# Optimization experiments

Measured on AMD Instinct MI355X. Metric: run time of the kernel, lower is better.

Reference implementation:

```python
import jax, jax.numpy as jnp
import numpy as np

BUCKET_SIZE = 64
N_HASHES = 8


def setup_inputs() -> dict:
    key = jax.random.key(0)
    ks = jax.random.split(key, 8)
    B, S, D = 4, 4096, 512
    n_buckets = S // BUCKET_SIZE  # 64
    x = jax.random.normal(ks[0], (B, S, D), dtype=jnp.float32)
    rotations = jax.random.normal(ks[1], (1, D, N_HASHES, n_buckets // 2), dtype=jnp.float32)
    w_qk = jax.random.normal(ks[2], (D, D), dtype=jnp.float32) * 0.02
    b_qk = jax.random.normal(ks[3], (D,), dtype=jnp.float32) * 0.02
    w_v = jax.random.normal(ks[4], (D, D), dtype=jnp.float32) * 0.02
    b_v = jax.random.normal(ks[5], (D,), dtype=jnp.float32) * 0.02
    w_out = jax.random.normal(ks[6], (D, D), dtype=jnp.float32) * 0.02
    b_out = jax.random.normal(ks[7], (D,), dtype=jnp.float32) * 0.02
    return {"x": x, "rotations": rotations, "w_qk": w_qk, "b_qk": b_qk,
            "w_v": w_v, "b_v": b_v, "w_out": w_out, "b_out": b_out}


def reference(x, rotations, w_qk, b_qk, w_v, b_v, w_out, b_out):
    B, S, D = x.shape
    T = S  # seqlen is already a multiple of 2*bucket_size -> no padding
    n_buckets = T // BUCKET_SIZE
    qk = x @ w_qk + b_qk            # [B, T, D]
    v = x @ w_v + b_v               # [B, T, D]

    # --- LSH bucketing ---
    rot = jnp.einsum('btf,fhi->bhti', qk, rotations[0])      # [B, H, T, nb/2]
    rot = jnp.concatenate([rot, -rot], axis=-1)              # [B, H, T, nb]
    buckets = jnp.argmax(rot, axis=-1)                       # [B, H, T]
    offsets = (jnp.arange(N_HASHES) * n_buckets)[None, :, None]
    buckets = (buckets + offsets).reshape(B, -1)             # [B, H*T]

    # --- stable sort by (bucket, position) ---
    ticker = jnp.arange(N_HASHES * T)[None, :]
    buckets_and_t = T * buckets + ticker % T                 # unique keys
    sticker = jnp.argsort(buckets_and_t, axis=-1)            # sorted ticker values
    undo_sort = jnp.argsort(sticker, axis=-1)
    st = sticker % T                                         # token positions

    # --- gather Q/K/V into sorted order ---
    idx = jnp.broadcast_to(st[:, :, None], (B, N_HASHES * T, D))
    sqk = jnp.take_along_axis(qk, idx, axis=1)               # [B, H*T, D]
    sv = jnp.take_along_axis(v, idx, axis=1)

    # --- chunked attention (no softmax, as in the original module) ---
    chunks = N_HASHES * n_buckets
    bq = sqk.reshape(B, chunks, BUCKET_SIZE, D)
    bv = sv.reshape(B, chunks, BUCKET_SIZE, D)
    norm = jnp.maximum(jnp.linalg.norm(bq, axis=-1, keepdims=True), 1e-12)
    bk = bq / norm                                           # F.normalize(p=2)
    dots = jnp.einsum('buie,buje->buij', bq, bk) * (D ** -0.5)
    bo = jnp.einsum('buij,buje->buie', dots, bv)             # [B, chunks, bs, D]

    # --- scatter back and combine hash rounds ---
    so = bo.reshape(B, -1, D)
    uidx = jnp.broadcast_to(undo_sort[:, :, None], (B, N_HASHES * T, D))
    o = jnp.take_along_axis(so, uidx, axis=1)
    out = o.reshape(B, N_HASHES, T, D).sum(axis=1)           # sum over hash rounds
    return out @ w_out + b_out
```

## Files before the change

kernel.cpp:

```cpp
#include <hip/hip_runtime.h>


typedef __attribute__((ext_vector_type(8))) short short8;
typedef __attribute__((ext_vector_type(4))) float f32x4;
typedef unsigned short ushort_t;

__device__ __forceinline__ ushort_t f2b(float f) {
  union { float f; unsigned u; } x; x.f = f;
  unsigned r = x.u + 0x7fffu + ((x.u >> 16) & 1u);
  return (ushort_t)(r >> 16);
}
__device__ __forceinline__ float b2f(unsigned b) {
  union { unsigned u; float f; } x; x.u = b << 16;
  return x.f;
}
__device__ __forceinline__ void gload16(void* lds, const void* gp) {
  __builtin_amdgcn_global_load_lds(
      (const __attribute__((address_space(1))) unsigned int*)gp,
      (__attribute__((address_space(3))) unsigned int*)lds, 16, 0, 0);
}

__global__ __launch_bounds__(256) void prep_kernel(
    const float* __restrict__ x, const float* __restrict__ w_qk,
    const float* __restrict__ b_qk, const float* __restrict__ R,
    const float* __restrict__ w_v, const float* __restrict__ w_out,
    ushort_t* __restrict__ xh, ushort_t* __restrict__ xl,
    ushort_t* __restrict__ wqkT, ushort_t* __restrict__ wvT, ushort_t* __restrict__ woT,
    ushort_t* __restrict__ W2Th, ushort_t* __restrict__ W2Tl, float* __restrict__ b2,
    int* __restrict__ mcount)
{
  __shared__ float t[32][33];
  __shared__ float wrow[512];
  const int blk = blockIdx.x, tid = threadIdx.x;
  if (blk == 0 && tid == 0) mcount[0] = 0;

  if (blk < 4096) {
    const int i = blk * 256 + tid;
    const float4 a = *(const float4*)(x + (size_t)i * 8);
    const float4 c = *(const float4*)(x + (size_t)i * 8 + 4);
    float v[8] = { a.x, a.y, a.z, a.w, c.x, c.y, c.z, c.w };
    ushort_t hi[8], lo[8];
    #pragma unroll
    for (int k = 0; k < 8; ++k) {
      hi[k] = f2b(v[k]);
      lo[k] = f2b(v[k] - b2f(hi[k]));
    }
    *(uint4*)(xh + (size_t)i * 8) = *(const uint4*)hi;
    *(uint4*)(xl + (size_t)i * 8) = *(const uint4*)lo;
  } else if (blk < 4864) {
    const int idx = blk - 4096;
    const int mat = idx >> 8, r = idx & 255;
    const float* W  = (mat == 0) ? w_qk : (mat == 1) ? w_v : w_out;
    ushort_t*   Wt  = (mat == 0) ? wqkT : (mat == 1) ? wvT : woT;
    const int bx = (r & 15) * 32, by = (r >> 4) * 32;
    const int tx = tid & 31, ty = tid >> 5;
    #pragma unroll
    for (int j = 0; j < 4; ++j)
      t[ty + j*8][tx] = W[(size_t)(by + ty + j*8) * 512 + bx + tx];
    __syncthreads();
    #pragma unroll
    for (int j = 0; j < 4; ++j)
      Wt[(size_t)(bx + ty + j*8) * 512 + by + tx] = f2b(t[tx][ty + j*8]);
  } else {
    const int e = blk - 4864, j = tid;
    const float* src = (e < 512) ? (w_qk + (size_t)e * 512) : b_qk;
    wrow[j]       = src[j];
    wrow[j + 256] = src[j + 256];
    __syncthreads();
    float acc = 0.f;
    for (int f = 0; f < 512; ++f)
      acc = fmaf(wrow[f], R[(size_t)f * 256 + j], acc);
    if (e < 512) {
      const ushort_t hi = f2b(acc);
      W2Th[(size_t)j * 512 + e] = hi;
      W2Tl[(size_t)j * 512 + e] = f2b(acc - b2f(hi));
    } else {
      b2[j] = acc;
    }
  }
}

__global__ __launch_bounds__(256, 2) void gemm_qkv(
    const ushort_t* __restrict__ A, const ushort_t* __restrict__ wqkT,
    const ushort_t* __restrict__ wvT, const float* __restrict__ b_qk,
    const float* __restrict__ b_v, ushort_t* __restrict__ qkv)
{
  __shared__ __align__(16) char Al[32768];
  __shared__ __align__(16) char Bl[32768];
  const int bm = blockIdx.x * 128;
  const int sel = blockIdx.y >> 2;
  const int bn = (blockIdx.y & 3) * 128;
  const ushort_t* Wt   = sel ? wvT : wqkT;
  const float*    bias = sel ? b_v : b_qk;
  const int coff = sel * 512;
  const int tid = threadIdx.x, w = tid >> 6, l = tid & 63;
  const int m = l & 15, gq = l >> 4;
  f32x4 acc[2][8] = {};

#define STAGE1(NB, K0) { \
    _Pragma("unroll") \
    for (int j = 0; j < 4; ++j) { \
      const int row = w * 32 + j * 8 + (l >> 3); \
      const int ch = (l & 7) ^ (row & 7); \
      const int dst = (NB) * 16384 + w * 4096 + j * 1024 + l * 16; \
      gload16(Al + dst, A  + (size_t)(bm + row) * 512 + (K0) + ch * 8); \
      gload16(Bl + dst, Wt + (size_t)(bn + row) * 512 + (K0) + ch * 8); \
    } }

  STAGE1(0, 0)
  __syncthreads();
  for (int t = 0; t < 8; ++t) {
    const int cur = t & 1;
    if (t < 7) STAGE1(cur ^ 1, (t + 1) * 64)
    #pragma unroll
    for (int ks = 0; ks < 2; ++ks) {
      short8 bfr[8];
      #pragma unroll
      for (int tj = 0; tj < 8; ++tj) {
        const int brow = tj * 16 + m;
        bfr[tj] = *(const short8*)(Bl + cur * 16384 + ((brow * 128 + ks * 64 + gq * 16) ^ ((brow & 7) << 4)));
      }
      #pragma unroll
      for (int ti = 0; ti < 2; ++ti) {
        const int arow = w * 32 + ti * 16 + m;
        const short8 af = *(const short8*)(Al + cur * 16384 + ((arow * 128 + ks * 64 + gq * 16) ^ ((arow & 7) << 4)));
        #pragma unroll
        for (int tj = 0; tj < 8; ++tj)
          acc[ti][tj] = __builtin_amdgcn_mfma_f32_16x16x32_bf16(af, bfr[tj], acc[ti][tj], 0, 0, 0);
      }
    }
    __syncthreads();
  }
#undef STAGE1
  #pragma unroll
  for (int ti = 0; ti < 2; ++ti)
    #pragma unroll
    for (int tj = 0; tj < 8; ++tj) {
      const int col = bn + tj * 16 + m;
      const float bvv = bias[col];
      #pragma unroll
      for (int r2 = 0; r2 < 4; ++r2) {
        const int row = bm + w * 32 + ti * 16 + gq * 4 + r2;
        qkv[(size_t)row * 1024 + coff + col] = f2b(acc[ti][tj][r2] + bvv);
      }
    }
}

__global__ __launch_bounds__(256, 2) void gemm_mfma(
    const ushort_t* __restrict__ A, const ushort_t* __restrict__ Wt,
    const float* __restrict__ bias, float* __restrict__ Cf)
{
  __shared__ __align__(16) char Al[32768];
  __shared__ __align__(16) char Bl[32768];
  const int bm = blockIdx.x * 128, bn = blockIdx.y * 128;
  const int tid = threadIdx.x, w = tid >> 6, l = tid & 63;
  const int m = l & 15, gq = l >> 4;
  f32x4 acc[2][8] = {};

#define STAGE1(NB, K0) { \
    _Pragma("unroll") \
    for (int j = 0; j < 4; ++j) { \
      const int row = w * 32 + j * 8 + (l >> 3); \
      const int ch = (l & 7) ^ (row & 7); \
      const int dst = (NB) * 16384 + w * 4096 + j * 1024 + l * 16; \
      gload16(Al + dst, A  + (size_t)(bm + row) * 512 + (K0) + ch * 8); \
      gload16(Bl + dst, Wt + (size_t)(bn + row) * 512 + (K0) + ch * 8); \
    } }

  STAGE1(0, 0)
  __syncthreads();
  for (int t = 0; t < 8; ++t) {
    const int cur = t & 1;
    if (t < 7) STAGE1(cur ^ 1, (t + 1) * 64)
    #pragma unroll
    for (int ks = 0; ks < 2; ++ks) {
      short8 bfr[8];
      #pragma unroll
      for (int tj = 0; tj < 8; ++tj) {
        const int brow = tj * 16 + m;
        bfr[tj] = *(const short8*)(Bl + cur * 16384 + ((brow * 128 + ks * 64 + gq * 16) ^ ((brow & 7) << 4)));
      }
      #pragma unroll
      for (int ti = 0; ti < 2; ++ti) {
        const int arow = w * 32 + ti * 16 + m;
        const short8 af = *(const short8*)(Al + cur * 16384 + ((arow * 128 + ks * 64 + gq * 16) ^ ((arow & 7) << 4)));
        #pragma unroll
        for (int tj = 0; tj < 8; ++tj)
          acc[ti][tj] = __builtin_amdgcn_mfma_f32_16x16x32_bf16(af, bfr[tj], acc[ti][tj], 0, 0, 0);
      }
    }
    __syncthreads();
  }
#undef STAGE1
  #pragma unroll
  for (int ti = 0; ti < 2; ++ti)
    #pragma unroll
    for (int tj = 0; tj < 8; ++tj) {
      const int col = bn + tj * 16 + m;
      const float bvv = bias[col];
      #pragma unroll
      for (int r2 = 0; r2 < 4; ++r2) {
        const int row = bm + w * 32 + ti * 16 + gq * 4 + r2;
        Cf[(size_t)row * 512 + col] = acc[ti][tj][r2] + bvv;
      }
    }
}

__global__ __launch_bounds__(256, 2) void rot3_mfma(
    const ushort_t* __restrict__ Ah, const ushort_t* __restrict__ Al,
    const ushort_t* __restrict__ Bh, const ushort_t* __restrict__ Bl,
    const float* __restrict__ b2, float* __restrict__ rot)
{
  __shared__ __align__(16) char AH[16384], AL[16384], BH[16384], BL[16384];
  const int bm = blockIdx.x * 128, bn = blockIdx.y * 128;
  const int tid = threadIdx.x, w = tid >> 6, l = tid & 63;
  const int m = l & 15, gq = l >> 4;
  f32x4 acc[2][8] = {};
  for (int k0 = 0; k0 < 512; k0 += 64) {
    #pragma unroll
    for (int j = 0; j < 4; ++j) {
      const int row = w * 32 + j * 8 + (l >> 3);
      const int ch = (l & 7) ^ (row & 7);
      const int dst = w * 4096 + j * 1024 + l * 16;
      gload16(AH + dst, Ah + (size_t)(bm + row) * 512 + k0 + ch * 8);
      gload16(AL + dst, Al + (size_t)(bm + row) * 512 + k0 + ch * 8);
      gload16(BH + dst, Bh + (size_t)(bn + row) * 512 + k0 + ch * 8);
      gload16(BL + dst, Bl + (size_t)(bn + row) * 512 + k0 + ch * 8);
    }
    __syncthreads();
    #pragma unroll
    for (int ks = 0; ks < 2; ++ks) {
      short8 bh8[8], bl8[8];
      #pragma unroll
      for (int tj = 0; tj < 8; ++tj) {
        const int ba = ((tj * 16 + m) * 128 + ks * 64 + gq * 16) ^ (((tj * 16 + m) & 7) << 4);
        bh8[tj] = *(const short8*)(BH + ba);
        bl8[tj] = *(const short8*)(BL + ba);
      }
      #pragma unroll
      for (int ti = 0; ti < 2; ++ti) {
        const int arow = w * 32 + ti * 16 + m;
        const int aa = (arow * 128 + ks * 64 + gq * 16) ^ ((arow & 7) << 4);
        const short8 ah8 = *(const short8*)(AH + aa);
        const short8 al8 = *(const short8*)(AL + aa);
        #pragma unroll
        for (int tj = 0; tj < 8; ++tj) {
          acc[ti][tj] = __builtin_amdgcn_mfma_f32_16x16x32_bf16(ah8, bh8[tj], acc[ti][tj], 0, 0, 0);
          acc[ti][tj] = __builtin_amdgcn_mfma_f32_16x16x32_bf16(al8, bh8[tj], acc[ti][tj], 0, 0, 0);
          acc[ti][tj] = __builtin_amdgcn_mfma_f32_16x16x32_bf16(ah8, bl8[tj], acc[ti][tj], 0, 0, 0);
        }
      }
    }
    __syncthreads();
  }
  #pragma unroll
  for (int ti = 0; ti < 2; ++ti)
    #pragma unroll
    for (int tj = 0; tj < 8; ++tj) {
      const int col = bn + tj * 16 + m;
      const float bvv = b2[col];
      #pragma unroll
      for (int r2 = 0; r2 < 4; ++r2) {
        const int row = bm + w * 32 + ti * 16 + gq * 4 + r2;
        rot[(size_t)row * 256 + col] = acc[ti][tj][r2] + bvv;
      }
    }
}

__global__ __launch_bounds__(256) void argmax_scale(
    const float* __restrict__ rot, int* __restrict__ buckets,
    int* __restrict__ mlist, int* __restrict__ mcount, float tau,
    const ushort_t* __restrict__ qkv, float* __restrict__ scale)
{
  const int blk = blockIdx.x;
  if (blk < 16384) {
    const int tok = blk;
    const int j = threadIdx.x;
    const float r = rot[(size_t)tok * 256 + j];
    float m1, m2; int i1;
    if (r >= 0.f) { m1 = r;  i1 = j & 31;        m2 = -r; }
    else          { m1 = -r; i1 = (j & 31) + 32; m2 = r;  }
    #pragma unroll
    for (int off = 16; off; off >>= 1) {
      const float om1 = __shfl_xor(m1, off);
      const int   oi1 = __shfl_xor(i1, off);
      const float om2 = __shfl_xor(m2, off);
      float loser;
      if (om1 > m1 || (om1 == m1 && oi1 < i1)) { loser = m1; m1 = om1; i1 = oi1; }
      else loser = om1;
      m2 = fmaxf(fmaxf(m2, om2), loser);
    }
    if ((j & 31) == 0) {
      const int h = j >> 5, b = tok >> 12, t = tok & 4095;
      buckets[((b << 3) + h) * 4096 + t] = i1;
      if (m1 - m2 < tau) {
        const int k = atomicAdd(mcount, 1);
        mlist[k] = (((b << 3) + h) << 12) | t;
      }
    }
  } else {
    const int wave = threadIdx.x >> 6, lane = threadIdx.x & 63;
    const int tok = (blk - 16384) * 4 + wave;
    const uint4 H = *(const uint4*)(qkv + (size_t)tok * 1024 + lane * 8);
    const unsigned* hp = (const unsigned*)&H;
    float s = 0.f;
    #pragma unroll
    for (int e = 0; e < 4; ++e) {
      const float v0 = b2f(hp[e] & 0xffffu);
      const float v1 = b2f(hp[e] >> 16);
      s += v0 * v0 + v1 * v1;
    }
    #pragma unroll
    for (int off = 32; off; off >>= 1) s += __shfl_down(s, off);
    if (lane == 0) {
      const float nn = fmaxf(sqrtf(s), 1e-12f);
      scale[tok] = 0.044194173824159216f / nn;
    }
  }
}

__global__ __launch_bounds__(512) void bucket_fallback(
    const float* __restrict__ x, const float* __restrict__ w_qk,
    const float* __restrict__ b_qk, const float* __restrict__ R,
    const int* __restrict__ mlist, const int* __restrict__ mcount,
    int* __restrict__ buckets)
{
  __shared__ float qkrow[512];
  const int n = mcount[0];
  for (int ii = blockIdx.x; ii < n; ii += gridDim.x) {
    const int mm = mlist[ii];
    const int bh = mm >> 12, t = mm & 4095;
    const int b = bh >> 3, h = bh & 7;
    const float* xr = x + ((size_t)b * 4096 + t) * 512;
    {
      const int c = threadIdx.x;
      float a0 = 0.f;
      for (int f = 0; f < 512; ++f) a0 = fmaf(xr[f], w_qk[(size_t)f * 512 + c], a0);
      qkrow[c] = a0 + b_qk[c];
    }
    __syncthreads();
    if (threadIdx.x < 32) {
      const int col = h * 32 + threadIdx.x;
      float a0 = 0.f;
      for (int f = 0; f < 512; ++f) a0 = fmaf(qkrow[f], R[(size_t)f * 256 + col], a0);
      float m1; int i1;
      if (a0 >= 0.f) { m1 = a0;  i1 = threadIdx.x; }
      else           { m1 = -a0; i1 = threadIdx.x + 32; }
      #pragma unroll
      for (int off = 16; off; off >>= 1) {
        const float om = __shfl_xor(m1, off);
        const int   oi = __shfl_xor(i1, off);
        if (om > m1 || (om == m1 && oi < i1)) { m1 = om; i1 = oi; }
      }
      if (threadIdx.x == 0) buckets[(size_t)bh * 4096 + t] = i1;
    }
    __syncthreads();
  }
}

__global__ __launch_bounds__(256) void sort_kernel(
    const int* __restrict__ buckets, int* __restrict__ st)
{
  __shared__ int bk_lds[4096];
  __shared__ int cnt[64][64];
  __shared__ int bstart[64];
  const int tid = threadIdx.x;
  const int base = blockIdx.x * 4096;
  const int wave = tid >> 6, lane = tid & 63;
  const unsigned long long lt = (1ull << lane) - 1ull;

  for (int t = tid; t < 4096; t += 256) bk_lds[t] = buckets[base + t];
  for (int i = tid; i < 4096; i += 256) ((int*)cnt)[i] = 0;
  __syncthreads();

  for (int c = wave; c < 64; c += 4) {
    const int bk = bk_lds[c * 64 + lane];
    unsigned long long mask = ~0ull;
    #pragma unroll
    for (int bit = 0; bit < 6; ++bit) {
      const unsigned long long bb = __ballot((bk >> bit) & 1);
      mask &= ((bk >> bit) & 1) ? bb : ~bb;
    }
    if ((mask & lt) == 0)
      cnt[c][bk] = __popcll(mask);
  }
  __syncthreads();

  if (tid < 64) {
    int run = 0;
    for (int c = 0; c < 64; ++c) {
      const int v = cnt[c][tid];
      cnt[c][tid] = run;
      run += v;
    }
    int ex = run;
    #pragma unroll
    for (int off = 1; off < 64; off <<= 1) {
      const int nn = __shfl_up(ex, off);
      if (lane >= off) ex += nn;
    }
    bstart[tid] = ex - run;
  }
  __syncthreads();

  for (int c = wave; c < 64; c += 4) {
    const int tok = c * 64 + lane;
    const int bk = bk_lds[tok];
    unsigned long long mask = ~0ull;
    #pragma unroll
    for (int bit = 0; bit < 6; ++bit) {
      const unsigned long long bb = __ballot((bk >> bit) & 1);
      mask &= ((bk >> bit) & 1) ? bb : ~bb;
    }
    const int rank = (int)__popcll(mask & lt);
    st[base + bstart[bk] + cnt[c][bk] + rank] = tok;
  }
}

__global__ __launch_bounds__(256, 2) void attn_mfma(
    const ushort_t* __restrict__ qkv, const float* __restrict__ scale,
    const int* __restrict__ st, ushort_t* __restrict__ so, int g, int hbase)
{
  __shared__ __align__(16) char Q[32768];
  __shared__ __align__(16) char VT[32768];
  __shared__ __align__(16) char P[8192];
  __shared__ int   stt[64];
  __shared__ float scl[64];

  const int blk = blockIdx.x;
  const int cpg = g * 64;
  const int b = blk / cpg, rem = blk % cpg;
  const int hl = rem >> 6, c = rem & 63;
  const int tid = threadIdx.x, w = tid >> 6, l = tid & 63;
  const int m = l & 15, gq = l >> 4;
  const int srow = tid >> 5, su = tid & 31;

  if (tid < 64) {
    const int s = st[(size_t)((b * 8 + hbase + hl) * 4096) + c * 64 + tid];
    stt[tid] = s;
    scl[tid] = scale[b * 4096 + s];
  }
  __syncthreads();

  const size_t qkbase = (size_t)b * 4096;
  uint4 rg[8];

#define LOADG(VOFF, HALF) { \
    _Pragma("unroll") \
    for (int it = 0; it < 8; ++it) { \
      const int row = it * 8 + srow; \
      rg[it] = *(const uint4*)(qkv + (qkbase + stt[row]) * 1024 + (VOFF) + (HALF) * 256 + su * 8); \
    } }
#define WRITEQ() { \
    _Pragma("unroll") \
    for (int it = 0; it < 8; ++it) { \
      const int row = it * 8 + srow; \
      *(uint4*)(Q + ((row * 512 + su * 16) ^ ((row & 7) << 4))) = rg[it]; \
    } }
#define WRITEVT() { \
    _Pragma("unroll") \
    for (int it = 0; it < 8; ++it) { \
      const int j = it * 8 + srow; \
      const ushort_t* e = (const ushort_t*)&rg[it]; \
      _Pragma("unroll") \
      for (int ee = 0; ee < 8; ++ee) { \
        const int d = su * 8 + ee; \
        *(ushort_t*)(VT + ((d * 128 + j * 2) ^ (((d ^ (d >> 3)) & 7) << 4))) = e[ee]; \
      } \
    } }
#define COMPUTE_S() { \
    _Pragma("unroll") \
    for (int kf = 0; kf < 8; ++kf) { \
      const int arow = w * 16 + m; \
      const short8 af = *(const short8*)(Q + ((arow * 512 + kf * 64 + gq * 16) ^ ((arow & 7) << 4))); \
      _Pragma("unroll") \
      for (int jt = 0; jt < 4; ++jt) { \
        const int brow = jt * 16 + m; \
        const short8 bf = *(const short8*)(Q + ((brow * 512 + kf * 64 + gq * 16) ^ ((brow & 7) << 4))); \
        accS[jt] = __builtin_amdgcn_mfma_f32_16x16x32_bf16(af, bf, accS[jt], 0, 0, 0); \
      } \
    } }
#define COMPUTE_PV(ACCO) { \
    _Pragma("unroll") \
    for (int dt = 0; dt < 16; ++dt) { \
      _Pragma("unroll") \
      for (int kf = 0; kf < 2; ++kf) { \
        const int d = dt * 16 + m; \
        const short8 bv = *(const short8*)(VT + ((d * 128 + kf * 64 + gq * 16) ^ (((d ^ (d >> 3)) & 7) << 4))); \
        ACCO[dt] = __builtin_amdgcn_mfma_f32_16x16x32_bf16(ap[kf], bv, ACCO[dt], 0, 0, 0); \
      } \
    } }
#define BOUNCE(ACCO) { \
    _Pragma("unroll") \
    for (int dt = 0; dt < 16; ++dt) \
      _Pragma("unroll") \
      for (int r = 0; r < 4; ++r) { \
        const int i = w * 16 + gq * 4 + r; \
        const int dcol = dt * 16 + m; \
        *(ushort_t*)(Q + ((i * 512 + dcol * 2) ^ ((i & 7) << 4))) = f2b(ACCO[dt][r]); \
      } }
#define FLUSH(HALF) { \
    _Pragma("unroll") \
    for (int it = 0; it < 8; ++it) { \
      const int row = it * 8 + srow; \
      const uint4 dat = *(const uint4*)(Q + ((row * 512 + su * 16) ^ ((row & 7) << 4))); \
      *(uint4*)(so + (sobase + stt[row]) * 512 + (HALF) * 256 + su * 8) = dat; \
    } }

  f32x4 accS[4] = {};

  LOADG(0, 0)
  WRITEQ()
  __syncthreads();
  LOADG(0, 1)
  COMPUTE_S()
  __syncthreads();
  WRITEQ()
  __syncthreads();
  LOADG(512, 0)
  COMPUTE_S()
  __syncthreads();

  #pragma unroll
  for (int jt = 0; jt < 4; ++jt)
    #pragma unroll
    for (int r = 0; r < 4; ++r) {
      const int i = w * 16 + gq * 4 + r;
      const int j = jt * 16 + m;
      *(ushort_t*)(P + ((i * 128 + j * 2) ^ ((i & 7) << 4))) = f2b(accS[jt][r] * scl[j]);
    }
  WRITEVT()
  __syncthreads();

  const size_t sobase = (size_t)(b * g + hl) * 4096;
  LOADG(512, 1)
  short8 ap[2];
  #pragma unroll
  for (int kf = 0; kf < 2; ++kf) {
    const int i = w * 16 + m;
    ap[kf] = *(const short8*)(P + ((i * 128 + kf * 64 + gq * 16) ^ ((i & 7) << 4)));
  }
  f32x4 accO[16] = {};
  COMPUTE_PV(accO)
  __syncthreads();

  WRITEVT()
  BOUNCE(accO)
  __syncthreads();

  FLUSH(0)
  f32x4 accO2[16] = {};
  COMPUTE_PV(accO2)
  __syncthreads();

  BOUNCE(accO2)
  __syncthreads();
  FLUSH(1)

#undef LOADG
#undef WRITEQ
#undef WRITEVT
#undef COMPUTE_S
#undef COMPUTE_PV
#undef BOUNCE
#undef FLUSH
}

__global__ __launch_bounds__(256) void gather_kernel(
    const ushort_t* __restrict__ so, ushort_t* __restrict__ o_b, int g, int first)
{
  const int tok = blockIdx.x;
  const int b = tok >> 12, t = tok & 4095;
  const int d0 = threadIdx.x * 2;
  ushort_t* dst = o_b + (size_t)tok * 512 + d0;
  float ax = 0.f, ay = 0.f;
  if (!first) {
    const unsigned u = *(const unsigned*)dst;
    ax = b2f(u & 0xffffu); ay = b2f(u >> 16);
  }
  const size_t stride = (size_t)4096 * 512;
  const ushort_t* src = so + ((size_t)(b * g) * 4096 + t) * 512 + d0;
  for (int hlp = 0; hlp < g; ++hlp) {
    const unsigned u = *(const unsigned*)src;
    ax += b2f(u & 0xffffu);
    ay += b2f(u >> 16);
    src += stride;
  }
  *(unsigned*)dst = ((unsigned)f2b(ay) << 16) | (unsigned)f2b(ax);
}

extern "C" void kernel_launch(void* const* d_in, const int* in_sizes, int n_in,
                              void* d_out, int out_size, void* d_ws, size_t ws_size,
                              hipStream_t stream) {
  const float* x         = (const float*)d_in[0];
  const float* rotations = (const float*)d_in[1];
  const float* w_qk      = (const float*)d_in[2];
  const float* b_qk      = (const float*)d_in[3];
  const float* w_v       = (const float*)d_in[4];
  const float* b_v       = (const float*)d_in[5];
  const float* w_out     = (const float*)d_in[6];
  const float* b_out     = (const float*)d_in[7];
  float* out = (float*)d_out;
  char* ws = (char*)d_ws;

  ushort_t* xh      = (ushort_t*)(ws);
  ushort_t* xl      = (ushort_t*)(ws + 16777216);
  ushort_t* qkv     = (ushort_t*)(ws + 33554432);
  float*    rot     = (float*)(ws + 67108864);
  ushort_t* o_b     = (ushort_t*)(ws + 67108864);
  ushort_t* wqkTh   = (ushort_t*)(ws + 83886080);
  ushort_t* wvT     = (ushort_t*)(ws + 84410368);
  ushort_t* woT     = (ushort_t*)(ws + 84934656);
  ushort_t* W2Th    = (ushort_t*)(ws + 85458944);
  ushort_t* W2Tl    = (ushort_t*)(ws + 85721088);
  float*    b2      = (float*)(ws + 85983232);
  float*    scale   = (float*)(ws + 85987328);
  int*      buckets = (int*)(ws + 86052864);
  int*      st      = (int*)(ws + 86577152);
  int*      mlist   = (int*)(ws + 87101440);
  int*      mcount  = (int*)(ws + 87625728);
  ushort_t* so      = (ushort_t*)(ws + 87629824);
  const size_t so_off = 87629824;

  int g = 1;
  for (int cand = 8; cand >= 1; cand >>= 1)
    if (so_off + (size_t)cand * 16777216ull <= ws_size) { g = cand; break; }

  const dim3 blk256(256);
  hipLaunchKernelGGL(prep_kernel, dim3(5377), blk256, 0, stream,
                     x, w_qk, b_qk, rotations, w_v, w_out,
                     xh, xl, wqkTh, wvT, woT, W2Th, W2Tl, b2, mcount);

  hipLaunchKernelGGL(gemm_qkv, dim3(128, 8), blk256, 0, stream, xh, wqkTh, wvT, b_qk, b_v, qkv);
  hipLaunchKernelGGL(rot3_mfma, dim3(128, 2), blk256, 0, stream, xh, xl, W2Th, W2Tl, b2, rot);

  hipLaunchKernelGGL(argmax_scale, dim3(20480), blk256, 0, stream,
                     rot, buckets, mlist, mcount, 1.5e-3f, qkv, scale);
  hipLaunchKernelGGL(bucket_fallback, dim3(1024), dim3(512), 0, stream,
                     x, w_qk, b_qk, rotations, mlist, mcount, buckets);
  hipLaunchKernelGGL(sort_kernel, dim3(32), blk256, 0, stream, buckets, st);

  const int passes = 8 / g;
  for (int p = 0; p < passes; ++p) {
    const int hbase = p * g;
    hipLaunchKernelGGL(attn_mfma, dim3(4 * g * 64), blk256, 0, stream,
                       qkv, scale, st, so, g, hbase);
    hipLaunchKernelGGL(gather_kernel, dim3(16384), blk256, 0, stream,
                       so, o_b, g, (p == 0) ? 1 : 0);
  }

  hipLaunchKernelGGL(gemm_mfma, dim3(128, 4), blk256, 0, stream, o_b, woT, b_out, out);
}
```

Before: 244.4 us.

## Merge QKV and rotation GEMMs into one launch; raise MFMA wave priority in attention

The QKV projection GEMM and the split-precision rotation GEMM now run as one kernel with a 128x10 grid. The first eight grid rows do the QKV tiles and the last two do the rotation tiles, sharing one 64KB LDS buffer. This removes a kernel launch and lets the small rotation GEMM (256 blocks) overlap with the QKV blocks instead of running as a separate under-filled wave. Separately, the attention kernel brackets its MFMA loops with s_setprio so waves issuing matrix ops get scheduling priority over waves doing loads.

```diff
diff --git a/kernel.cpp b/kernel.cpp
--- a/kernel.cpp
+++ b/kernel.cpp
@@ -80,22 +80,28 @@
   }
 }
 
-__global__ __launch_bounds__(256, 2) void gemm_qkv(
-    const ushort_t* __restrict__ A, const ushort_t* __restrict__ wqkT,
-    const ushort_t* __restrict__ wvT, const float* __restrict__ b_qk,
-    const float* __restrict__ b_v, ushort_t* __restrict__ qkv)
-{
-  __shared__ __align__(16) char Al[32768];
-  __shared__ __align__(16) char Bl[32768];
+__global__ __launch_bounds__(256, 2) void gemm_qkvr(
+    const ushort_t* __restrict__ A, const ushort_t* __restrict__ Axl,
+    const ushort_t* __restrict__ wqkT, const ushort_t* __restrict__ wvT,
+    const float* __restrict__ b_qk, const float* __restrict__ b_v,
+    ushort_t* __restrict__ qkv,
+    const ushort_t* __restrict__ W2Th, const ushort_t* __restrict__ W2Tl,
+    const float* __restrict__ b2, float* __restrict__ rot)
+{
+  __shared__ __align__(16) char lds[65536];
   const int bm = blockIdx.x * 128;
-  const int sel = blockIdx.y >> 2;
-  const int bn = (blockIdx.y & 3) * 128;
-  const ushort_t* Wt   = sel ? wvT : wqkT;
-  const float*    bias = sel ? b_v : b_qk;
-  const int coff = sel * 512;
   const int tid = threadIdx.x, w = tid >> 6, l = tid & 63;
   const int m = l & 15, gq = l >> 4;
-  f32x4 acc[2][8] = {};
+
+  if (blockIdx.y < 8) {
+    char* Al = lds;
+    char* Bl = lds + 32768;
+    const int sel = blockIdx.y >> 2;
+    const int bn = (blockIdx.y & 3) * 128;
+    const ushort_t* Wt   = sel ? wvT : wqkT;
+    const float*    bias = sel ? b_v : b_qk;
+    const int coff = sel * 512;
+    f32x4 acc[2][8] = {};
 
 #define STAGE1(NB, K0) { \
     _Pragma("unroll") \
@@ -107,43 +113,100 @@
       gload16(Bl + dst, Wt + (size_t)(bn + row) * 512 + (K0) + ch * 8); \
     } }
 
-  STAGE1(0, 0)
-  __syncthreads();
-  for (int t = 0; t < 8; ++t) {
-    const int cur = t & 1;
-    if (t < 7) STAGE1(cur ^ 1, (t + 1) * 64)
-    #pragma unroll
-    for (int ks = 0; ks < 2; ++ks) {
-      short8 bfr[8];
+    STAGE1(0, 0)
+    __syncthreads();
+    for (int t = 0; t < 8; ++t) {
+      const int cur = t & 1;
+      if (t < 7) STAGE1(cur ^ 1, (t + 1) * 64)
+      #pragma unroll
+      for (int ks = 0; ks < 2; ++ks) {
+        short8 bfr[8];
+        #pragma unroll
+        for (int tj = 0; tj < 8; ++tj) {
+          const int brow = tj * 16 + m;
+          bfr[tj] = *(const short8*)(Bl + cur * 16384 + ((brow * 128 + ks * 64 + gq * 16) ^ ((brow & 7) << 4)));
+        }
+        #pragma unroll
+        for (int ti = 0; ti < 2; ++ti) {
+          const int arow = w * 32 + ti * 16 + m;
+          const short8 af = *(const short8*)(Al + cur * 16384 + ((arow * 128 + ks * 64 + gq * 16) ^ ((arow & 7) << 4)));
+          #pragma unroll
+          for (int tj = 0; tj < 8; ++tj)
+            acc[ti][tj] = __builtin_amdgcn_mfma_f32_16x16x32_bf16(af, bfr[tj], acc[ti][tj], 0, 0, 0);
+        }
+      }
+      __syncthreads();
+    }
+#undef STAGE1
+    #pragma unroll
+    for (int ti = 0; ti < 2; ++ti)
       #pragma unroll
       for (int tj = 0; tj < 8; ++tj) {
-        const int brow = tj * 16 + m;
-        bfr[tj] = *(const short8*)(Bl + cur * 16384 + ((brow * 128 + ks * 64 + gq * 16) ^ ((brow & 7) << 4)));
-      }
-      #pragma unroll
-      for (int ti = 0; ti < 2; ++ti) {
-        const int arow = w * 32 + ti * 16 + m;
-        const short8 af = *(const short8*)(Al + cur * 16384 + ((arow * 128 + ks * 64 + gq * 16) ^ ((arow & 7) << 4)));
+        const int col = bn + tj * 16 + m;
+        const float bvv = bias[col];
         #pragma unroll
-        for (int tj = 0; tj < 8; ++tj)
-          acc[ti][tj] = __builtin_amdgcn_mfma_f32_16x16x32_bf16(af, bfr[tj], acc[ti][tj], 0, 0, 0);
-      }
-    }
-    __syncthreads();
-  }
-#undef STAGE1
-  #pragma unroll
-  for (int ti = 0; ti < 2; ++ti)
-    #pragma unroll
-    for (int tj = 0; tj < 8; ++tj) {
-      const int col = bn + tj * 16 + m;
-      const float bvv = bias[col];
-      #pragma unroll
-      for (int r2 = 0; r2 < 4; ++r2) {
-        const int row = bm + w * 32 + ti * 16 + gq * 4 + r2;
-        qkv[(size_t)row * 1024 + coff + col] = f2b(acc[ti][tj][r2] + bvv);
-      }
-    }
+        for (int r2 = 0; r2 < 4; ++r2) {
+          const int row = bm + w * 32 + ti * 16 + gq * 4 + r2;
+          qkv[(size_t)row * 1024 + coff + col] = f2b(acc[ti][tj][r2] + bvv);
+        }
+      }
+  } else {
+    char* AH = lds;
+    char* AL = lds + 16384;
+    char* BH = lds + 32768;
+    char* BL = lds + 49152;
+    const int bn = (blockIdx.y - 8) * 128;
+    f32x4 acc[2][8] = {};
+    for (int k0 = 0; k0 < 512; k0 += 64) {
+      #pragma unroll
+      for (int j = 0; j < 4; ++j) {
+        const int row = w * 32 + j * 8 + (l >> 3);
+        const int ch = (l & 7) ^ (row & 7);
+        const int dst = w * 4096 + j * 1024 + l * 16;
+        gload16(AH + dst, A    + (size_t)(bm + row) * 512 + k0 + ch * 8);
+        gload16(AL + dst, Axl  + (size_t)(bm + row) * 512 + k0 + ch * 8);
+        gload16(BH + dst, W2Th + (size_t)(bn + row) * 512 + k0 + ch * 8);
+        gload16(BL + dst, W2Tl + (size_t)(bn + row) * 512 + k0 + ch * 8);
+      }
+      __syncthreads();
+      #pragma unroll
+      for (int ks = 0; ks < 2; ++ks) {
+        short8 bh8[8], bl8[8];
+        #pragma unroll
+        for (int tj = 0; tj < 8; ++tj) {
+          const int ba = ((tj * 16 + m) * 128 + ks * 64 + gq * 16) ^ (((tj * 16 + m) & 7) << 4);
+          bh8[tj] = *(const short8*)(BH + ba);
+          bl8[tj] = *(const short8*)(BL + ba);
+        }
+        #pragma unroll
+        for (int ti = 0; ti < 2; ++ti) {
+          const int arow = w * 32 + ti * 16 + m;
+          const int aa = (arow * 128 + ks * 64 + gq * 16) ^ ((arow & 7) << 4);
+          const short8 ah8 = *(const short8*)(AH + aa);
+          const short8 al8 = *(const short8*)(AL + aa);
+          #pragma unroll
+          for (int tj = 0; tj < 8; ++tj) {
+            acc[ti][tj] = __builtin_amdgcn_mfma_f32_16x16x32_bf16(ah8, bh8[tj], acc[ti][tj], 0, 0, 0);
+            acc[ti][tj] = __builtin_amdgcn_mfma_f32_16x16x32_bf16(al8, bh8[tj], acc[ti][tj], 0, 0, 0);
+            acc[ti][tj] = __builtin_amdgcn_mfma_f32_16x16x32_bf16(ah8, bl8[tj], acc[ti][tj], 0, 0, 0);
+          }
+        }
+      }
+      __syncthreads();
+    }
+    #pragma unroll
+    for (int ti = 0; ti < 2; ++ti)
+      #pragma unroll
+      for (int tj = 0; tj < 8; ++tj) {
+        const int col = bn + tj * 16 + m;
+        const float bvv = b2[col];
+        #pragma unroll
+        for (int r2 = 0; r2 < 4; ++r2) {
+          const int row = bm + w * 32 + ti * 16 + gq * 4 + r2;
+          rot[(size_t)row * 256 + col] = acc[ti][tj][r2] + bvv;
+        }
+      }
+  }
 }
 
 __global__ __launch_bounds__(256, 2) void gemm_mfma(
@@ -202,67 +265,6 @@
       for (int r2 = 0; r2 < 4; ++r2) {
         const int row = bm + w * 32 + ti * 16 + gq * 4 + r2;
         Cf[(size_t)row * 512 + col] = acc[ti][tj][r2] + bvv;
-      }
-    }
-}
-
-__global__ __launch_bounds__(256, 2) void rot3_mfma(
-    const ushort_t* __restrict__ Ah, const ushort_t* __restrict__ Al,
-    const ushort_t* __restrict__ Bh, const ushort_t* __restrict__ Bl,
-    const float* __restrict__ b2, float* __restrict__ rot)
-{
-  __shared__ __align__(16) char AH[16384], AL[16384], BH[16384], BL[16384];
-  const int bm = blockIdx.x * 128, bn = blockIdx.y * 128;
-  const int tid = threadIdx.x, w = tid >> 6, l = tid & 63;
-  const int m = l & 15, gq = l >> 4;
-  f32x4 acc[2][8] = {};
-  for (int k0 = 0; k0 < 512; k0 += 64) {
-    #pragma unroll
-    for (int j = 0; j < 4; ++j) {
-      const int row = w * 32 + j * 8 + (l >> 3);
-      const int ch = (l & 7) ^ (row & 7);
-      const int dst = w * 4096 + j * 1024 + l * 16;
-      gload16(AH + dst, Ah + (size_t)(bm + row) * 512 + k0 + ch * 8);
-      gload16(AL + dst, Al + (size_t)(bm + row) * 512 + k0 + ch * 8);
-      gload16(BH + dst, Bh + (size_t)(bn + row) * 512 + k0 + ch * 8);
-      gload16(BL + dst, Bl + (size_t)(bn + row) * 512 + k0 + ch * 8);
-    }
-    __syncthreads();
-    #pragma unroll
-    for (int ks = 0; ks < 2; ++ks) {
-      short8 bh8[8], bl8[8];
-      #pragma unroll
-      for (int tj = 0; tj < 8; ++tj) {
-        const int ba = ((tj * 16 + m) * 128 + ks * 64 + gq * 16) ^ (((tj * 16 + m) & 7) << 4);
-        bh8[tj] = *(const short8*)(BH + ba);
-        bl8[tj] = *(const short8*)(BL + ba);
-      }
-      #pragma unroll
-      for (int ti = 0; ti < 2; ++ti) {
-        const int arow = w * 32 + ti * 16 + m;
-        const int aa = (arow * 128 + ks * 64 + gq * 16) ^ ((arow & 7) << 4);
-        const short8 ah8 = *(const short8*)(AH + aa);
-        const short8 al8 = *(const short8*)(AL + aa);
-        #pragma unroll
-        for (int tj = 0; tj < 8; ++tj) {
-          acc[ti][tj] = __builtin_amdgcn_mfma_f32_16x16x32_bf16(ah8, bh8[tj], acc[ti][tj], 0, 0, 0);
-          acc[ti][tj] = __builtin_amdgcn_mfma_f32_16x16x32_bf16(al8, bh8[tj], acc[ti][tj], 0, 0, 0);
-          acc[ti][tj] = __builtin_amdgcn_mfma_f32_16x16x32_bf16(ah8, bl8[tj], acc[ti][tj], 0, 0, 0);
-        }
-      }
-    }
-    __syncthreads();
-  }
-  #pragma unroll
-  for (int ti = 0; ti < 2; ++ti)
-    #pragma unroll
-    for (int tj = 0; tj < 8; ++tj) {
-      const int col = bn + tj * 16 + m;
-      const float bvv = b2[col];
-      #pragma unroll
-      for (int r2 = 0; r2 < 4; ++r2) {
-        const int row = bm + w * 32 + ti * 16 + gq * 4 + r2;
-        rot[(size_t)row * 256 + col] = acc[ti][tj][r2] + bvv;
       }
     }
 }
@@ -469,6 +471,7 @@
       } \
     } }
 #define COMPUTE_S() { \
+    __builtin_amdgcn_s_setprio(1); \
     _Pragma("unroll") \
     for (int kf = 0; kf < 8; ++kf) { \
       const int arow = w * 16 + m; \
@@ -479,8 +482,10 @@
         const short8 bf = *(const short8*)(Q + ((brow * 512 + kf * 64 + gq * 16) ^ ((brow & 7) << 4))); \
         accS[jt] = __builtin_amdgcn_mfma_f32_16x16x32_bf16(af, bf, accS[jt], 0, 0, 0); \
       } \
-    } }
+    } \
+    __builtin_amdgcn_s_setprio(0); }
 #define COMPUTE_PV(ACCO) { \
+    __builtin_amdgcn_s_setprio(1); \
     _Pragma("unroll") \
     for (int dt = 0; dt < 16; ++dt) { \
       _Pragma("unroll") \
@@ -489,7 +494,8 @@
         const short8 bv = *(const short8*)(VT + ((d * 128 + kf * 64 + gq * 16) ^ (((d ^ (d >> 3)) & 7) << 4))); \
         ACCO[dt] = __builtin_amdgcn_mfma_f32_16x16x32_bf16(ap[kf], bv, ACCO[dt], 0, 0, 0); \
       } \
-    } }
+    } \
+    __builtin_amdgcn_s_setprio(0); }
 #define BOUNCE(ACCO) { \
     _Pragma("unroll") \
     for (int dt = 0; dt < 16; ++dt) \
@@ -631,8 +637,8 @@
                      x, w_qk, b_qk, rotations, w_v, w_out,
                      xh, xl, wqkTh, wvT, woT, W2Th, W2Tl, b2, mcount);
 
-  hipLaunchKernelGGL(gemm_qkv, dim3(128, 8), blk256, 0, stream, xh, wqkTh, wvT, b_qk, b_v, qkv);
-  hipLaunchKernelGGL(rot3_mfma, dim3(128, 2), blk256, 0, stream, xh, xl, W2Th, W2Tl, b2, rot);
+  hipLaunchKernelGGL(gemm_qkvr, dim3(128, 10), blk256, 0, stream,
+                     xh, xl, wqkTh, wvT, b_qk, b_v, qkv, W2Th, W2Tl, b2, rot);
 
   hipLaunchKernelGGL(argmax_scale, dim3(20480), blk256, 0, stream,
                      rot, buckets, mlist, mcount, 1.5e-3f, qkv, scale);
```

New measurement: 249.8 us. +2.2%, slower.
